# Performance work log

Hardware: AMD Instinct MI355X
Metric: run time of the kernel (lower is better)

## Reference

```python
import jax, jax.numpy as jnp
import numpy as np

E = 768
H_HEADS = 12


def trilinear_border_sample(feat_map, coords):
    """grid_sample 3D, mode='bilinear', padding_mode='border', align_corners=True.
    feat_map: (B, C, D, H, W); coords: (B, P, 3) in [-1,1], last dim = (x, y, z) -> (W, H, D).
    Returns (B, P, C).
    """
    B, C, D, H, W = feat_map.shape
    x, y, z = coords[..., 0], coords[..., 1], coords[..., 2]
    ix = (x + 1.0) * 0.5 * (W - 1)
    iy = (y + 1.0) * 0.5 * (H - 1)
    iz = (z + 1.0) * 0.5 * (D - 1)
    x0 = jnp.floor(ix); y0 = jnp.floor(iy); z0 = jnp.floor(iz)
    wx = ix - x0; wy = iy - y0; wz = iz - z0
    x0i = jnp.clip(x0, 0, W - 1).astype(jnp.int32)
    x1i = jnp.clip(x0 + 1, 0, W - 1).astype(jnp.int32)
    y0i = jnp.clip(y0, 0, H - 1).astype(jnp.int32)
    y1i = jnp.clip(y0 + 1, 0, H - 1).astype(jnp.int32)
    z0i = jnp.clip(z0, 0, D - 1).astype(jnp.int32)
    z1i = jnp.clip(z0 + 1, 0, D - 1).astype(jnp.int32)
    flat = feat_map.reshape(B, C, D * H * W)

    def gather(zi, yi, xi):
        idx = (zi * H + yi) * W + xi  # (B, P)
        return jnp.take_along_axis(flat, idx[:, None, :], axis=2)  # (B, C, P)

    out = (
        gather(z0i, y0i, x0i) * ((1 - wz) * (1 - wy) * (1 - wx))[:, None, :]
        + gather(z0i, y0i, x1i) * ((1 - wz) * (1 - wy) * wx)[:, None, :]
        + gather(z0i, y1i, x0i) * ((1 - wz) * wy * (1 - wx))[:, None, :]
        + gather(z0i, y1i, x1i) * ((1 - wz) * wy * wx)[:, None, :]
        + gather(z1i, y0i, x0i) * (wz * (1 - wy) * (1 - wx))[:, None, :]
        + gather(z1i, y0i, x1i) * (wz * (1 - wy) * wx)[:, None, :]
        + gather(z1i, y1i, x0i) * (wz * wy * (1 - wx))[:, None, :]
        + gather(z1i, y1i, x1i) * (wz * wy * wx)[:, None, :]
    )
    return out.transpose(0, 2, 1)  # (B, P, C)


def setup_inputs() -> dict:
    key = jax.random.key(0)
    ks = jax.random.split(key, 12)
    B, fullN, nb = 64, 513, 32
    s = 1.0 / np.sqrt(E)
    return {
        "x": jax.random.normal(ks[0], (B, fullN, E), jnp.float32),
        "bio_embed": jax.random.normal(ks[1], (B, E), jnp.float32),
        "base_coords": jax.random.uniform(ks[2], (nb, 3), jnp.float32),
        "offsets": jax.random.normal(ks[3], (B, nb, 3), jnp.float32) * 0.1,
        "confidence": jax.random.uniform(ks[4], (B, 1), jnp.float32),
        "sample_proj_w": jax.random.uniform(ks[5], (E, E), jnp.float32, -s, s),
        "sample_proj_b": jax.random.uniform(ks[6], (E,), jnp.float32, -s, s),
        "in_proj_w": jax.random.uniform(ks[7], (3 * E, E), jnp.float32, -s, s),
        "in_proj_b": jnp.zeros((3 * E,), jnp.float32),
        "out_proj_w": jax.random.uniform(ks[8], (E, E), jnp.float32, -s, s),
        "out_proj_b": jnp.zeros((E,), jnp.float32),
        "grid_size": 8,
    }


def reference(x, bio_embed, base_coords, offsets, confidence,
              sample_proj_w, sample_proj_b, in_proj_w, in_proj_b,
              out_proj_w, out_proj_b, grid_size):
    B, fullN, C = x.shape
    G = grid_size
    patch_tokens = x[:, 1:, :]  # (B, N, C), N = G^3
    feat_map = patch_tokens.transpose(0, 2, 1).reshape(B, C, G, G, G)

    coords = jnp.clip(base_coords[None, :, :] + offsets, -1.0, 1.0)  # (B, nb, 3)
    sampled = trilinear_border_sample(feat_map, coords)  # (B, nb, C)
    sampled = sampled @ sample_proj_w.T + sample_proj_b

    # MultiheadAttention: single query (bio_embed), keys/values = sampled tokens
    hd = E // H_HEADS
    Wq, Wk, Wv = in_proj_w[:E], in_proj_w[E:2 * E], in_proj_w[2 * E:]
    bq, bk, bv = in_proj_b[:E], in_proj_b[E:2 * E], in_proj_b[2 * E:]
    q = (bio_embed @ Wq.T + bq).reshape(B, H_HEADS, hd)
    k = (sampled @ Wk.T + bk).reshape(B, -1, H_HEADS, hd)
    v = (sampled @ Wv.T + bv).reshape(B, -1, H_HEADS, hd)
    scores = jnp.einsum('bhd,bphd->bhp', q, k) / jnp.sqrt(jnp.asarray(hd, q.dtype))
    attn = jax.nn.softmax(scores, axis=-1)
    ctx = jnp.einsum('bhp,bphd->bhd', attn, v).reshape(B, E)
    attn_out = ctx @ out_proj_w.T + out_proj_b  # (B, E)

    out = jnp.broadcast_to(attn_out[:, None, :], (B, fullN, C))
    out = out * confidence[:, :, None]
    return out
```

## Files before the change

kernel.cpp:

```cpp
#include <hip/hip_runtime.h>
#include <hip/hip_bf16.h>
#include <math.h>

#define E 768
#define NH 12
#define HD 64

typedef __attribute__((ext_vector_type(8))) short bf16x8;
typedef __attribute__((ext_vector_type(4))) float f32x4;

__device__ __forceinline__ unsigned short f2bf_rne(float f) {
    unsigned int u = __float_as_uint(f);
    u += 0x7FFF + ((u >> 16) & 1);
    return (unsigned short)(u >> 16);
}

__global__ __launch_bounds__(256) void fused_conv_sample(
    const float* __restrict__ spw, const float* __restrict__ ipw,
    const float* __restrict__ x,
    const float* __restrict__ bcrd, const float* __restrict__ offs,
    const int* __restrict__ gsize,
    const float* __restrict__ bio, const float* __restrict__ ipb,
    unsigned short* __restrict__ spw_bf, unsigned short* __restrict__ kvw_bf,
    unsigned short* __restrict__ sampled, float* __restrict__ qout,
    int B, int P, int fullN, int nb_conv1, int nb_conv2)
{
    int blk = blockIdx.x;
    int t = threadIdx.x;

    if (blk < nb_conv1) {
        int i = blk * 256 + t;
        float4 v = ((const float4*)spw)[i];
        ushort4 o;
        o.x = f2bf_rne(v.x); o.y = f2bf_rne(v.y);
        o.z = f2bf_rne(v.z); o.w = f2bf_rne(v.w);
        ((ushort4*)spw_bf)[i] = o;
        return;
    }
    blk -= nb_conv1;
    if (blk < nb_conv2) {
        int i = blk * 256 + t;
        float4 v = ((const float4*)(ipw + (size_t)E * E))[i];
        ushort4 o;
        o.x = f2bf_rne(v.x); o.y = f2bf_rne(v.y);
        o.z = f2bf_rne(v.z); o.w = f2bf_rne(v.w);
        ((ushort4*)kvw_bf)[i] = o;
        return;
    }
    blk -= nb_conv2;
    if (blk < B * P) {
        int bp = blk;
        int b = bp / P, p = bp % P;
        int G = *gsize;
        float gm1 = (float)(G - 1);

        float cx = bcrd[p * 3 + 0] + offs[bp * 3 + 0];
        float cy = bcrd[p * 3 + 1] + offs[bp * 3 + 1];
        float cz = bcrd[p * 3 + 2] + offs[bp * 3 + 2];
        cx = fminf(fmaxf(cx, -1.f), 1.f);
        cy = fminf(fmaxf(cy, -1.f), 1.f);
        cz = fminf(fmaxf(cz, -1.f), 1.f);

        float ix = (cx + 1.f) * 0.5f * gm1;
        float iy = (cy + 1.f) * 0.5f * gm1;
        float iz = (cz + 1.f) * 0.5f * gm1;
        float fx = floorf(ix), fy = floorf(iy), fz = floorf(iz);
        float wx = ix - fx, wy = iy - fy, wz = iz - fz;

        int x0 = (int)fminf(fmaxf(fx,       0.f), gm1);
        int x1 = (int)fminf(fmaxf(fx + 1.f, 0.f), gm1);
        int y0 = (int)fminf(fmaxf(fy,       0.f), gm1);
        int y1 = (int)fminf(fmaxf(fy + 1.f, 0.f), gm1);
        int z0 = (int)fminf(fmaxf(fz,       0.f), gm1);
        int z1 = (int)fminf(fmaxf(fz + 1.f, 0.f), gm1);

        int tk[8];
        tk[0] = (z0 * G + y0) * G + x0;
        tk[1] = (z0 * G + y0) * G + x1;
        tk[2] = (z0 * G + y1) * G + x0;
        tk[3] = (z0 * G + y1) * G + x1;
        tk[4] = (z1 * G + y0) * G + x0;
        tk[5] = (z1 * G + y0) * G + x1;
        tk[6] = (z1 * G + y1) * G + x0;
        tk[7] = (z1 * G + y1) * G + x1;
        float wgt[8];
        wgt[0] = (1.f - wz) * (1.f - wy) * (1.f - wx);
        wgt[1] = (1.f - wz) * (1.f - wy) * wx;
        wgt[2] = (1.f - wz) * wy * (1.f - wx);
        wgt[3] = (1.f - wz) * wy * wx;
        wgt[4] = wz * (1.f - wy) * (1.f - wx);
        wgt[5] = wz * (1.f - wy) * wx;
        wgt[6] = wz * wy * (1.f - wx);
        wgt[7] = wz * wy * wx;

        const float4* xb4 = (const float4*)(x + ((size_t)b * fullN + 1) * E);
        ushort4* outp = (ushort4*)(sampled + (size_t)bp * E);
        for (int c4 = t; c4 < E / 4; c4 += 256) {
            float4 acc = {0.f, 0.f, 0.f, 0.f};
#pragma unroll
            for (int k = 0; k < 8; ++k) {
                float4 v = xb4[(size_t)tk[k] * (E / 4) + c4];
                acc.x += wgt[k] * v.x; acc.y += wgt[k] * v.y;
                acc.z += wgt[k] * v.z; acc.w += wgt[k] * v.w;
            }
            ushort4 o;
            o.x = f2bf_rne(acc.x); o.y = f2bf_rne(acc.y);
            o.z = f2bf_rne(acc.z); o.w = f2bf_rne(acc.w);
            outp[c4] = o;
        }
        return;
    }
    blk -= B * P;
    {
        int wid = blk * 4 + (t >> 6);
        int ln = t & 63;
        if (wid >= B * E) return;
        int m = wid / E, n = wid % E;
        const float* a = bio + (size_t)m * E;
        const float* w = ipw + (size_t)n * E;
        float s = 0.f;
        for (int k = ln; k < E; k += 64) s += a[k] * w[k];
#pragma unroll
        for (int off = 32; off; off >>= 1) s += __shfl_down(s, off);
        if (ln == 0) qout[wid] = s + ipb[n];
    }
}

template <bool OUT_BF16>
__global__ __launch_bounds__(256) void gemm64_bf16_nt(
    const unsigned short* __restrict__ A,
    const unsigned short* __restrict__ W,
    const float* __restrict__ bias,
    void* __restrict__ C,
    int M, int N, int K)
{
    __shared__ unsigned short lsA[64 * 32];
    __shared__ unsigned short lsB[64 * 32];

    int wv = threadIdx.x >> 6;
    int ln = threadIdx.x & 63;
    int m0 = blockIdx.y * 64;
    int n0 = blockIdx.x * 64;
    int wm = (wv & 1) * 32;
    int wn = (wv >> 1) * 32;

    f32x4 acc[2][2] = {};

    int srow = ln >> 2;
    int scol = (ln & 3) * 8;

    for (int k0 = 0; k0 < K; k0 += 32) {
        int row = wv * 16 + srow;
        const unsigned short* ga = A + (size_t)(m0 + row) * K + k0 + scol;
        const unsigned short* gw = W + (size_t)(n0 + row) * K + k0 + scol;
        __builtin_amdgcn_global_load_lds(
            (const __attribute__((address_space(1))) unsigned int*)ga,
            (__attribute__((address_space(3))) unsigned int*)(lsA + wv * 16 * 32),
            16, 0, 0);
        __builtin_amdgcn_global_load_lds(
            (const __attribute__((address_space(1))) unsigned int*)gw,
            (__attribute__((address_space(3))) unsigned int*)(lsB + wv * 16 * 32),
            16, 0, 0);
        __syncthreads();

        int kq = (ln >> 4) * 8;
        int rsel = ln & 15;
        bf16x8 af[2], bfr[2];
#pragma unroll
        for (int i = 0; i < 2; ++i) {
            af[i]  = *(const bf16x8*)&lsA[(wm + i * 16 + rsel) * 32 + kq];
            bfr[i] = *(const bf16x8*)&lsB[(wn + i * 16 + rsel) * 32 + kq];
        }
#pragma unroll
        for (int i = 0; i < 2; ++i)
#pragma unroll
            for (int j = 0; j < 2; ++j)
                acc[i][j] = __builtin_amdgcn_mfma_f32_16x16x32_bf16(
                    af[i], bfr[j], acc[i][j], 0, 0, 0);
        __syncthreads();
    }

    int cr = (ln >> 4) * 4;
    int cc = ln & 15;
#pragma unroll
    for (int j = 0; j < 2; ++j) {
        int col = n0 + wn + j * 16 + cc;
        float bv = bias[col];
#pragma unroll
        for (int i = 0; i < 2; ++i) {
#pragma unroll
            for (int r = 0; r < 4; ++r) {
                int row = m0 + wm + i * 16 + cr + r;
                float v = acc[i][j][r] + bv;
                if (OUT_BF16)
                    ((unsigned short*)C)[(size_t)row * N + col] = f2bf_rne(v);
                else
                    ((float*)C)[(size_t)row * N + col] = v;
            }
        }
    }
}

__global__ void matvec_nt(const float* __restrict__ A,
                          const float* __restrict__ W,
                          const float* __restrict__ bias,
                          float* __restrict__ C,
                          int M, int N, int K)
{
    int wid = blockIdx.x * (blockDim.x >> 6) + (threadIdx.x >> 6);
    int ln = threadIdx.x & 63;
    if (wid >= M * N) return;
    int m = wid / N, n = wid % N;
    const float* a = A + (size_t)m * K;
    const float* w = W + (size_t)n * K;
    float s = 0.f;
    for (int k = ln; k < K; k += 64) s += a[k] * w[k];
#pragma unroll
    for (int off = 32; off; off >>= 1) s += __shfl_down(s, off);
    if (ln == 0) C[wid] = s + bias[n];
}

__global__ void attn_kernel(const float* __restrict__ q,
                            const float* __restrict__ kv,
                            float* __restrict__ ctx,
                            int B, int P)
{
    int bh = blockIdx.x;
    int b = bh / NH, h = bh % NH;
    int d = threadIdx.x;

    __shared__ float qs[HD];
    __shared__ float sc[64];

    qs[d] = q[(size_t)b * E + h * HD + d];
    __syncthreads();

    if (d < P) {
        const float* kr = kv + ((size_t)(b * P + d)) * (2 * E) + h * HD;
        float s = 0.f;
#pragma unroll
        for (int e = 0; e < HD; ++e) s += qs[e] * kr[e];
        sc[d] = s * 0.125f;
    }
    __syncthreads();

    float mx = -INFINITY;
    for (int p = 0; p < P; ++p) mx = fmaxf(mx, sc[p]);
    float den = 0.f;
    for (int p = 0; p < P; ++p) den += __expf(sc[p] - mx);
    __syncthreads();
    if (d < P) sc[d] = __expf(sc[d] - mx) / den;
    __syncthreads();

    float acc = 0.f;
    for (int p = 0; p < P; ++p)
        acc += sc[p] * kv[((size_t)(b * P + p)) * (2 * E) + E + h * HD + d];
    ctx[(size_t)b * E + h * HD + d] = acc;
}

__global__ void bcast_kernel(const float* __restrict__ attn_out,
                             const float* __restrict__ conf,
                             float* __restrict__ out,
                             int fullN, int pc)
{
    int b = blockIdx.y;
    float cf = conf[b];
    const float4* ao = (const float4*)(attn_out + (size_t)b * E);
    float4* ob = (float4*)(out + (size_t)b * fullN * E);
    int i = blockIdx.x * blockDim.x + threadIdx.x;
    if (i < pc) {
        int c4 = i % (E / 4);
        float4 v = ao[c4];
        v.x *= cf; v.y *= cf; v.z *= cf; v.w *= cf;
        ob[i] = v;
    }
}

extern "C" void kernel_launch(void* const* d_in, const int* in_sizes, int n_in,
                              void* d_out, int out_size, void* d_ws, size_t ws_size,
                              hipStream_t stream)
{
    const float* x      = (const float*)d_in[0];
    const float* bio    = (const float*)d_in[1];
    const float* bcrd   = (const float*)d_in[2];
    const float* offs   = (const float*)d_in[3];
    const float* conf   = (const float*)d_in[4];
    const float* spw    = (const float*)d_in[5];
    const float* spb    = (const float*)d_in[6];
    const float* ipw    = (const float*)d_in[7];
    const float* ipb    = (const float*)d_in[8];
    const float* opw    = (const float*)d_in[9];
    const float* opb    = (const float*)d_in[10];
    const int*   gsize  = (const int*)d_in[11];
    float* out = (float*)d_out;

    const int B     = in_sizes[1] / E;
    const int P     = in_sizes[2] / 3;
    const int fullN = in_sizes[0] / (B * E);
    const int M     = B * P;

    char* base = (char*)d_out;
    unsigned short* sampled_bf = (unsigned short*)(base + 0);
    unsigned short* sproj_bf   = (unsigned short*)(base + 3145728);
    unsigned short* spw_bf     = (unsigned short*)(base + 6291456);
    unsigned short* ipwkv_bf   = (unsigned short*)(base + 7471104);
    float*          kv         = (float*)(base + 9830400);
    float*          q          = (float*)(base + 22413312);
    float*          ctx        = (float*)(base + 22609920);
    float*          aout       = (float*)d_ws;

    int nb_conv1 = (E * E) / 1024;
    int nb_conv2 = (2 * E * E) / 1024;
    int nb_q     = (B * E + 3) / 4;
    int nblocks  = nb_conv1 + nb_conv2 + M + nb_q;
    fused_conv_sample<<<nblocks, 256, 0, stream>>>(spw, ipw, x, bcrd, offs, gsize,
                                                   bio, ipb,
                                                   spw_bf, ipwkv_bf, sampled_bf, q,
                                                   B, P, fullN, nb_conv1, nb_conv2);

    gemm64_bf16_nt<true><<<dim3(E / 64, M / 64), 256, 0, stream>>>(
        sampled_bf, spw_bf, spb, sproj_bf, M, E, E);

    gemm64_bf16_nt<false><<<dim3(2 * E / 64, M / 64), 256, 0, stream>>>(
        sproj_bf, ipwkv_bf, ipb + E, kv, M, 2 * E, E);

    attn_kernel<<<B * NH, 64, 0, stream>>>(q, kv, ctx, B, P);

    {
        int tot = B * E;
        matvec_nt<<<(tot + 3) / 4, 256, 0, stream>>>(ctx, opw, opb, aout, B, E, E);
    }

    int pc = fullN * E / 4;
    bcast_kernel<<<dim3((pc + 255) / 256, B), 256, 0, stream>>>(aout, conf, out, fullN, pc);
}
```

Before: 289.9 us.

## Fuse all stages into a cooperative persistent megakernel with grid syncs

```diff
diff --git a/kernel.cpp b/kernel.cpp
--- a/kernel.cpp
+++ b/kernel.cpp
@@ -1,10 +1,14 @@
 #include <hip/hip_runtime.h>
+#include <hip/hip_cooperative_groups.h>
 #include <hip/hip_bf16.h>
 #include <math.h>
+
+namespace cg = cooperative_groups;
 
 #define E 768
 #define NH 12
 #define HD 64
+#define NTHR 256
 
 typedef __attribute__((ext_vector_type(8))) short bf16x8;
 typedef __attribute__((ext_vector_type(4))) float f32x4;
@@ -15,132 +19,79 @@
     return (unsigned short)(u >> 16);
 }
 
-__global__ __launch_bounds__(256) void fused_conv_sample(
-    const float* __restrict__ spw, const float* __restrict__ ipw,
-    const float* __restrict__ x,
-    const float* __restrict__ bcrd, const float* __restrict__ offs,
-    const int* __restrict__ gsize,
-    const float* __restrict__ bio, const float* __restrict__ ipb,
-    unsigned short* __restrict__ spw_bf, unsigned short* __restrict__ kvw_bf,
-    unsigned short* __restrict__ sampled, float* __restrict__ qout,
-    int B, int P, int fullN, int nb_conv1, int nb_conv2)
-{
-    int blk = blockIdx.x;
-    int t = threadIdx.x;
-
-    if (blk < nb_conv1) {
-        int i = blk * 256 + t;
-        float4 v = ((const float4*)spw)[i];
+
+__device__ __forceinline__ void sample_one(
+    const float* x, const float* bcrd, const float* offs, int G,
+    unsigned short* sampled, int u, int P, int fullN, int t, int tstep)
+{
+    int b = u / P, p = u % P;
+    float gm1 = (float)(G - 1);
+
+    float cx = bcrd[p * 3 + 0] + offs[u * 3 + 0];
+    float cy = bcrd[p * 3 + 1] + offs[u * 3 + 1];
+    float cz = bcrd[p * 3 + 2] + offs[u * 3 + 2];
+    cx = fminf(fmaxf(cx, -1.f), 1.f);
+    cy = fminf(fmaxf(cy, -1.f), 1.f);
+    cz = fminf(fmaxf(cz, -1.f), 1.f);
+
+    float ix = (cx + 1.f) * 0.5f * gm1;
+    float iy = (cy + 1.f) * 0.5f * gm1;
+    float iz = (cz + 1.f) * 0.5f * gm1;
+    float fx = floorf(ix), fy = floorf(iy), fz = floorf(iz);
+    float wx = ix - fx, wy = iy - fy, wz = iz - fz;
+
+    int x0 = (int)fminf(fmaxf(fx,       0.f), gm1);
+    int x1 = (int)fminf(fmaxf(fx + 1.f, 0.f), gm1);
+    int y0 = (int)fminf(fmaxf(fy,       0.f), gm1);
+    int y1 = (int)fminf(fmaxf(fy + 1.f, 0.f), gm1);
+    int z0 = (int)fminf(fmaxf(fz,       0.f), gm1);
+    int z1 = (int)fminf(fmaxf(fz + 1.f, 0.f), gm1);
+
+    int tk[8];
+    tk[0] = (z0 * G + y0) * G + x0;
+    tk[1] = (z0 * G + y0) * G + x1;
+    tk[2] = (z0 * G + y1) * G + x0;
+    tk[3] = (z0 * G + y1) * G + x1;
+    tk[4] = (z1 * G + y0) * G + x0;
+    tk[5] = (z1 * G + y0) * G + x1;
+    tk[6] = (z1 * G + y1) * G + x0;
+    tk[7] = (z1 * G + y1) * G + x1;
+    float wgt[8];
+    wgt[0] = (1.f - wz) * (1.f - wy) * (1.f - wx);
+    wgt[1] = (1.f - wz) * (1.f - wy) * wx;
+    wgt[2] = (1.f - wz) * wy * (1.f - wx);
+    wgt[3] = (1.f - wz) * wy * wx;
+    wgt[4] = wz * (1.f - wy) * (1.f - wx);
+    wgt[5] = wz * (1.f - wy) * wx;
+    wgt[6] = wz * wy * (1.f - wx);
+    wgt[7] = wz * wy * wx;
+
+    const float4* xb4 = (const float4*)(x + ((size_t)b * fullN + 1) * E);
+    ushort4* outp = (ushort4*)(sampled + (size_t)u * E);
+    for (int c4 = t; c4 < E / 4; c4 += tstep) {
+        float4 acc = {0.f, 0.f, 0.f, 0.f};
+#pragma unroll
+        for (int k = 0; k < 8; ++k) {
+            float4 v = xb4[(size_t)tk[k] * (E / 4) + c4];
+            acc.x += wgt[k] * v.x; acc.y += wgt[k] * v.y;
+            acc.z += wgt[k] * v.z; acc.w += wgt[k] * v.w;
+        }
         ushort4 o;
-        o.x = f2bf_rne(v.x); o.y = f2bf_rne(v.y);
-        o.z = f2bf_rne(v.z); o.w = f2bf_rne(v.w);
-        ((ushort4*)spw_bf)[i] = o;
-        return;
-    }
-    blk -= nb_conv1;
-    if (blk < nb_conv2) {
-        int i = blk * 256 + t;
-        float4 v = ((const float4*)(ipw + (size_t)E * E))[i];
-        ushort4 o;
-        o.x = f2bf_rne(v.x); o.y = f2bf_rne(v.y);
-        o.z = f2bf_rne(v.z); o.w = f2bf_rne(v.w);
-        ((ushort4*)kvw_bf)[i] = o;
-        return;
-    }
-    blk -= nb_conv2;
-    if (blk < B * P) {
-        int bp = blk;
-        int b = bp / P, p = bp % P;
-        int G = *gsize;
-        float gm1 = (float)(G - 1);
-
-        float cx = bcrd[p * 3 + 0] + offs[bp * 3 + 0];
-        float cy = bcrd[p * 3 + 1] + offs[bp * 3 + 1];
-        float cz = bcrd[p * 3 + 2] + offs[bp * 3 + 2];
-        cx = fminf(fmaxf(cx, -1.f), 1.f);
-        cy = fminf(fmaxf(cy, -1.f), 1.f);
-        cz = fminf(fmaxf(cz, -1.f), 1.f);
-
-        float ix = (cx + 1.f) * 0.5f * gm1;
-        float iy = (cy + 1.f) * 0.5f * gm1;
-        float iz = (cz + 1.f) * 0.5f * gm1;
-        float fx = floorf(ix), fy = floorf(iy), fz = floorf(iz);
-        float wx = ix - fx, wy = iy - fy, wz = iz - fz;
-
-        int x0 = (int)fminf(fmaxf(fx,       0.f), gm1);
-        int x1 = (int)fminf(fmaxf(fx + 1.f, 0.f), gm1);
-        int y0 = (int)fminf(fmaxf(fy,       0.f), gm1);
-        int y1 = (int)fminf(fmaxf(fy + 1.f, 0.f), gm1);
-        int z0 = (int)fminf(fmaxf(fz,       0.f), gm1);
-        int z1 = (int)fminf(fmaxf(fz + 1.f, 0.f), gm1);
-
-        int tk[8];
-        tk[0] = (z0 * G + y0) * G + x0;
-        tk[1] = (z0 * G + y0) * G + x1;
-        tk[2] = (z0 * G + y1) * G + x0;
-        tk[3] = (z0 * G + y1) * G + x1;
-        tk[4] = (z1 * G + y0) * G + x0;
-        tk[5] = (z1 * G + y0) * G + x1;
-        tk[6] = (z1 * G + y1) * G + x0;
-        tk[7] = (z1 * G + y1) * G + x1;
-        float wgt[8];
-        wgt[0] = (1.f - wz) * (1.f - wy) * (1.f - wx);
-        wgt[1] = (1.f - wz) * (1.f - wy) * wx;
-        wgt[2] = (1.f - wz) * wy * (1.f - wx);
-        wgt[3] = (1.f - wz) * wy * wx;
-        wgt[4] = wz * (1.f - wy) * (1.f - wx);
-        wgt[5] = wz * (1.f - wy) * wx;
-        wgt[6] = wz * wy * (1.f - wx);
-        wgt[7] = wz * wy * wx;
-
-        const float4* xb4 = (const float4*)(x + ((size_t)b * fullN + 1) * E);
-        ushort4* outp = (ushort4*)(sampled + (size_t)bp * E);
-        for (int c4 = t; c4 < E / 4; c4 += 256) {
-            float4 acc = {0.f, 0.f, 0.f, 0.f};
-#pragma unroll
-            for (int k = 0; k < 8; ++k) {
-                float4 v = xb4[(size_t)tk[k] * (E / 4) + c4];
-                acc.x += wgt[k] * v.x; acc.y += wgt[k] * v.y;
-                acc.z += wgt[k] * v.z; acc.w += wgt[k] * v.w;
-            }
-            ushort4 o;
-            o.x = f2bf_rne(acc.x); o.y = f2bf_rne(acc.y);
-            o.z = f2bf_rne(acc.z); o.w = f2bf_rne(acc.w);
-            outp[c4] = o;
-        }
-        return;
-    }
-    blk -= B * P;
-    {
-        int wid = blk * 4 + (t >> 6);
-        int ln = t & 63;
-        if (wid >= B * E) return;
-        int m = wid / E, n = wid % E;
-        const float* a = bio + (size_t)m * E;
-        const float* w = ipw + (size_t)n * E;
-        float s = 0.f;
-        for (int k = ln; k < E; k += 64) s += a[k] * w[k];
-#pragma unroll
-        for (int off = 32; off; off >>= 1) s += __shfl_down(s, off);
-        if (ln == 0) qout[wid] = s + ipb[n];
+        o.x = f2bf_rne(acc.x); o.y = f2bf_rne(acc.y);
+        o.z = f2bf_rne(acc.z); o.w = f2bf_rne(acc.w);
+        outp[c4] = o;
     }
 }
 
 template <bool OUT_BF16>
-__global__ __launch_bounds__(256) void gemm64_bf16_nt(
-    const unsigned short* __restrict__ A,
-    const unsigned short* __restrict__ W,
-    const float* __restrict__ bias,
-    void* __restrict__ C,
-    int M, int N, int K)
-{
-    __shared__ unsigned short lsA[64 * 32];
-    __shared__ unsigned short lsB[64 * 32];
-
+__device__ __forceinline__ void gemm64_tile(
+    const unsigned short* A, const unsigned short* W,
+    const float* bias, void* C,
+    int N, int K, int m0, int n0,
+    unsigned short* lsA, unsigned short* lsB)
+{
     int wv = threadIdx.x >> 6;
     int ln = threadIdx.x & 63;
-    int m0 = blockIdx.y * 64;
-    int n0 = blockIdx.x * 64;
     int wm = (wv & 1) * 32;
     int wn = (wv >> 1) * 32;
 
@@ -201,61 +152,221 @@
     }
 }
 
-__global__ void matvec_nt(const float* __restrict__ A,
-                          const float* __restrict__ W,
-                          const float* __restrict__ bias,
-                          float* __restrict__ C,
-                          int M, int N, int K)
-{
-    int wid = blockIdx.x * (blockDim.x >> 6) + (threadIdx.x >> 6);
-    int ln = threadIdx.x & 63;
-    if (wid >= M * N) return;
-    int m = wid / N, n = wid % N;
+__device__ __forceinline__ void matvec_wave(
+    const float* A, const float* W, const float* bias, float* C,
+    int u, int N, int K, int ln)
+{
+    int m = u / N, n = u % N;
     const float* a = A + (size_t)m * K;
     const float* w = W + (size_t)n * K;
     float s = 0.f;
     for (int k = ln; k < K; k += 64) s += a[k] * w[k];
 #pragma unroll
     for (int off = 32; off; off >>= 1) s += __shfl_down(s, off);
-    if (ln == 0) C[wid] = s + bias[n];
-}
-
-__global__ void attn_kernel(const float* __restrict__ q,
-                            const float* __restrict__ kv,
-                            float* __restrict__ ctx,
-                            int B, int P)
-{
-    int bh = blockIdx.x;
-    int b = bh / NH, h = bh % NH;
-    int d = threadIdx.x;
-
-    __shared__ float qs[HD];
-    __shared__ float sc[64];
-
-    qs[d] = q[(size_t)b * E + h * HD + d];
-    __syncthreads();
-
-    if (d < P) {
-        const float* kr = kv + ((size_t)(b * P + d)) * (2 * E) + h * HD;
-        float s = 0.f;
-#pragma unroll
-        for (int e = 0; e < HD; ++e) s += qs[e] * kr[e];
-        sc[d] = s * 0.125f;
-    }
-    __syncthreads();
-
-    float mx = -INFINITY;
-    for (int p = 0; p < P; ++p) mx = fmaxf(mx, sc[p]);
-    float den = 0.f;
-    for (int p = 0; p < P; ++p) den += __expf(sc[p] - mx);
-    __syncthreads();
-    if (d < P) sc[d] = __expf(sc[d] - mx) / den;
-    __syncthreads();
+    if (ln == 0) C[u] = s + bias[n];
+}
+
+__device__ __forceinline__ void attn_wave(
+    const float* q, const float* kv, float* ctx, int u, int P, int ln)
+{
+    int b = u / NH, h = u % NH;
+    float qd = q[(size_t)b * E + h * HD + ln];
+    const float* kvb = kv + (size_t)b * P * (2 * E);
+
+    int krow = (ln < P) ? ln : 0;
+    const float* kr = kvb + (size_t)krow * (2 * E) + h * HD;
+    float accd = 0.f;
+#pragma unroll
+    for (int e = 0; e < HD; ++e) accd += __shfl(qd, e) * kr[e];
+    float s = (ln < P) ? accd * 0.125f : -INFINITY;
+
+    float mx = s;
+#pragma unroll
+    for (int off = 32; off; off >>= 1) mx = fmaxf(mx, __shfl_xor(mx, off));
+    float ex = (ln < P) ? __expf(s - mx) : 0.f;
+    float den = ex;
+#pragma unroll
+    for (int off = 32; off; off >>= 1) den += __shfl_xor(den, off);
+    float pl = ex / den;
 
     float acc = 0.f;
     for (int p = 0; p < P; ++p)
-        acc += sc[p] * kv[((size_t)(b * P + p)) * (2 * E) + E + h * HD + d];
-    ctx[(size_t)b * E + h * HD + d] = acc;
+        acc += __shfl(pl, p) * kvb[(size_t)p * (2 * E) + E + h * HD + ln];
+    ctx[(size_t)b * E + h * HD + ln] = acc;
+}
+
+__global__ __launch_bounds__(256, 2) void mega(
+    const float* __restrict__ x, const float* __restrict__ bio,
+    const float* __restrict__ bcrd, const float* __restrict__ offs,
+    const float* __restrict__ conf,
+    const float* __restrict__ spw, const float* __restrict__ spb,
+    const float* __restrict__ ipw, const float* __restrict__ ipb,
+    const float* __restrict__ opw, const float* __restrict__ opb,
+    const int* __restrict__ gsize,
+    float* out,
+    unsigned short* sampled_bf, unsigned short* sproj_bf,
+    unsigned short* spw_bf, unsigned short* kvw_bf,
+    float* kv, float* q, float* ctx, float* aout,
+    int B, int P, int fullN)
+{
+    cg::grid_group grid = cg::this_grid();
+
+    __shared__ unsigned short lsA[64 * 32];
+    __shared__ unsigned short lsB[64 * 32];
+
+    const int bid  = blockIdx.x;
+    const int t    = threadIdx.x;
+    const int nblk = gridDim.x;
+    const int tid  = bid * NTHR + t;
+    const int nthr = nblk * NTHR;
+    const int wid  = tid >> 6;
+    const int nwav = nthr >> 6;
+    const int ln   = t & 63;
+    const int M    = B * P;
+
+    for (int i = tid; i < E * E / 4; i += nthr) {
+        float4 v = ((const float4*)spw)[i];
+        ushort4 o;
+        o.x = f2bf_rne(v.x); o.y = f2bf_rne(v.y);
+        o.z = f2bf_rne(v.z); o.w = f2bf_rne(v.w);
+        ((ushort4*)spw_bf)[i] = o;
+    }
+    for (int i = tid; i < 2 * E * E / 4; i += nthr) {
+        float4 v = ((const float4*)(ipw + (size_t)E * E))[i];
+        ushort4 o;
+        o.x = f2bf_rne(v.x); o.y = f2bf_rne(v.y);
+        o.z = f2bf_rne(v.z); o.w = f2bf_rne(v.w);
+        ((ushort4*)kvw_bf)[i] = o;
+    }
+    for (int u = wid; u < B * E; u += nwav)
+        matvec_wave(bio, ipw, ipb, q, u, E, E, ln);
+    {
+        int G = *gsize;
+        for (int u = bid; u < M; u += nblk)
+            sample_one(x, bcrd, offs, G, sampled_bf, u, P, fullN, t, NTHR);
+    }
+
+    grid.sync();
+
+    {
+        const int ntN = E / 64;
+        const int ntiles = (M / 64) * ntN;
+        for (int u = bid; u < ntiles; u += nblk)
+            gemm64_tile<true>(sampled_bf, spw_bf, spb, sproj_bf,
+                              E, E, (u / ntN) * 64, (u % ntN) * 64, lsA, lsB);
+    }
+
+    grid.sync();
+
+    {
+        const int ntN = 2 * E / 64;
+        const int ntiles = (M / 64) * ntN;
+        for (int u = bid; u < ntiles; u += nblk)
+            gemm64_tile<false>(sproj_bf, kvw_bf, ipb + E, kv,
+                               2 * E, E, (u / ntN) * 64, (u % ntN) * 64, lsA, lsB);
+    }
+
+    grid.sync();
+
+    for (int u = wid; u < B * NH; u += nwav)
+        attn_wave(q, kv, ctx, u, P, ln);
+
+    grid.sync();
+
+    for (int u = wid; u < B * E; u += nwav)
+        matvec_wave(ctx, opw, opb, aout, u, E, E, ln);
+
+    grid.sync();
+
+    {
+        int pc = fullN * E / 4;
+        for (int b = 0; b < B; ++b) {
+            float cf = conf[b];
+            const float4* ao = (const float4*)(aout + (size_t)b * E);
+            float4* ob = (float4*)(out + (size_t)b * fullN * E);
+            for (int i = tid; i < pc; i += nthr) {
+                int c4 = i % (E / 4);
+                float4 v = ao[c4];
+                v.x *= cf; v.y *= cf; v.z *= cf; v.w *= cf;
+                ob[i] = v;
+            }
+        }
+    }
+}
+
+__global__ __launch_bounds__(256) void fused_conv_sample(
+    const float* __restrict__ spw, const float* __restrict__ ipw,
+    const float* __restrict__ x,
+    const float* __restrict__ bcrd, const float* __restrict__ offs,
+    const int* __restrict__ gsize,
+    const float* __restrict__ bio, const float* __restrict__ ipb,
+    unsigned short* __restrict__ spw_bf, unsigned short* __restrict__ kvw_bf,
+    unsigned short* __restrict__ sampled, float* __restrict__ qout,
+    int B, int P, int fullN, int nb_conv1, int nb_conv2)
+{
+    int blk = blockIdx.x;
+    int t = threadIdx.x;
+
+    if (blk < nb_conv1) {
+        int i = blk * 256 + t;
+        float4 v = ((const float4*)spw)[i];
+        ushort4 o;
+        o.x = f2bf_rne(v.x); o.y = f2bf_rne(v.y);
+        o.z = f2bf_rne(v.z); o.w = f2bf_rne(v.w);
+        ((ushort4*)spw_bf)[i] = o;
+        return;
+    }
+    blk -= nb_conv1;
+    if (blk < nb_conv2) {
+        int i = blk * 256 + t;
+        float4 v = ((const float4*)(ipw + (size_t)E * E))[i];
+        ushort4 o;
+        o.x = f2bf_rne(v.x); o.y = f2bf_rne(v.y);
+        o.z = f2bf_rne(v.z); o.w = f2bf_rne(v.w);
+        ((ushort4*)kvw_bf)[i] = o;
+        return;
+    }
+    blk -= nb_conv2;
+    if (blk < B * P) {
+        sample_one(x, bcrd, offs, *gsize, sampled, blk, P, fullN, t, 256);
+        return;
+    }
+    blk -= B * P;
+    {
+        int u = blk * 4 + (t >> 6);
+        if (u < B * E) matvec_wave(bio, ipw, ipb, qout, u, E, E, t & 63);
+    }
+}
+
+template <bool OUT_BF16>
+__global__ __launch_bounds__(256) void gemm64_bf16_nt(
+    const unsigned short* __restrict__ A,
+    const unsigned short* __restrict__ W,
+    const float* __restrict__ bias,
+    void* __restrict__ C,
+    int M, int N, int K)
+{
+    __shared__ unsigned short lsA[64 * 32];
+    __shared__ unsigned short lsB[64 * 32];
+    gemm64_tile<OUT_BF16>(A, W, bias, C, N, K,
+                          blockIdx.y * 64, blockIdx.x * 64, lsA, lsB);
+}
+
+__global__ void attn_fb(const float* __restrict__ q,
+                        const float* __restrict__ kv,
+                        float* __restrict__ ctx, int B, int P)
+{
+    int u = blockIdx.x * 4 + (threadIdx.x >> 6);
+    if (u < B * NH) attn_wave(q, kv, ctx, u, P, threadIdx.x & 63);
+}
+
+__global__ void matvec_fb(const float* __restrict__ A,
+                          const float* __restrict__ W,
+                          const float* __restrict__ bias,
+                          float* __restrict__ C, int M, int N, int K)
+{
+    int u = blockIdx.x * 4 + (threadIdx.x >> 6);
+    if (u < M * N) matvec_wave(A, W, bias, C, u, N, K, threadIdx.x & 63);
 }
 
 __global__ void bcast_kernel(const float* __restrict__ attn_out,
@@ -294,20 +405,48 @@
     const int*   gsize  = (const int*)d_in[11];
     float* out = (float*)d_out;
 
-    const int B     = in_sizes[1] / E;
-    const int P     = in_sizes[2] / 3;
-    const int fullN = in_sizes[0] / (B * E);
-    const int M     = B * P;
+    int B     = in_sizes[1] / E;
+    int P     = in_sizes[2] / 3;
+    int fullN = in_sizes[0] / (B * E);
+    int M     = B * P;
 
     char* base = (char*)d_out;
     unsigned short* sampled_bf = (unsigned short*)(base + 0);
     unsigned short* sproj_bf   = (unsigned short*)(base + 3145728);
     unsigned short* spw_bf     = (unsigned short*)(base + 6291456);
-    unsigned short* ipwkv_bf   = (unsigned short*)(base + 7471104);
+    unsigned short* kvw_bf     = (unsigned short*)(base + 7471104);
     float*          kv         = (float*)(base + 9830400);
     float*          q          = (float*)(base + 22413312);
     float*          ctx        = (float*)(base + 22609920);
     float*          aout       = (float*)d_ws;
+
+    bool coop_done = false;
+    int maxBlocksPerCU = 0;
+    hipError_t oe = hipOccupancyMaxActiveBlocksPerMultiprocessor(
+        &maxBlocksPerCU, (const void*)mega, NTHR, 0);
+    if (oe == hipSuccess && maxBlocksPerCU >= 1) {
+        int nblk = maxBlocksPerCU * 256;
+        if (nblk > 768) nblk = 768;
+        void* kargs[] = {
+            (void*)&x, (void*)&bio, (void*)&bcrd, (void*)&offs, (void*)&conf,
+            (void*)&spw, (void*)&spb, (void*)&ipw, (void*)&ipb, (void*)&opw,
+            (void*)&opb, (void*)&gsize, (void*)&out,
+            (void*)&sampled_bf, (void*)&sproj_bf, (void*)&spw_bf, (void*)&kvw_bf,
+            (void*)&kv, (void*)&q, (void*)&ctx, (void*)&aout,
+            (void*)&B, (void*)&P, (void*)&fullN
+        };
+        hipError_t le = hipLaunchCooperativeKernel(
+            (const void*)mega, dim3(nblk), dim3(NTHR), kargs, 0, stream);
+        if (le == hipSuccess) {
+            coop_done = true;
+        } else {
+            (void)hipGetLastError();
+        }
+    } else {
+        (void)hipGetLastError();
+    }
+
+    if (coop_done) return;
 
     int nb_conv1 = (E * E) / 1024;
     int nb_conv2 = (2 * E * E) / 1024;
@@ -315,22 +454,14 @@
     int nblocks  = nb_conv1 + nb_conv2 + M + nb_q;
     fused_conv_sample<<<nblocks, 256, 0, stream>>>(spw, ipw, x, bcrd, offs, gsize,
                                                    bio, ipb,
-                                                   spw_bf, ipwkv_bf, sampled_bf, q,
+                                                   spw_bf, kvw_bf, sampled_bf, q,
                                                    B, P, fullN, nb_conv1, nb_conv2);
-
     gemm64_bf16_nt<true><<<dim3(E / 64, M / 64), 256, 0, stream>>>(
         sampled_bf, spw_bf, spb, sproj_bf, M, E, E);
-
     gemm64_bf16_nt<false><<<dim3(2 * E / 64, M / 64), 256, 0, stream>>>(
-        sproj_bf, ipwkv_bf, ipb + E, kv, M, 2 * E, E);
-
-    attn_kernel<<<B * NH, 64, 0, stream>>>(q, kv, ctx, B, P);
-
-    {
-        int tot = B * E;
-        matvec_nt<<<(tot + 3) / 4, 256, 0, stream>>>(ctx, opw, opb, aout, B, E, E);
-    }
-
+        sproj_bf, kvw_bf, ipb + E, kv, M, 2 * E, E);
+    attn_fb<<<(B * NH + 3) / 4, 256, 0, stream>>>(q, kv, ctx, B, P);
+    matvec_fb<<<(B * E + 3) / 4, 256, 0, stream>>>(ctx, opw, opb, aout, B, E, E);
     int pc = fullN * E / 4;
     bcast_kernel<<<dim3((pc + 255) / 256, B), 256, 0, stream>>>(aout, conf, out, fullN, pc);
 }
```

Result: slower. 725.7 us (+150.3%).
